# Performance work log

Measured on AMD Instinct MI355X. Metric: run time of the kernel, lower is better.

## Reference

```python
import jax, jax.numpy as jnp
import numpy as np

EPS = 1e-08


def setup_inputs() -> dict:
    key = jax.random.key(0)
    k1, k2 = jax.random.split(key)
    x = jax.random.normal(k1, (8192, 4096), dtype=jnp.float32)
    # xavier-uniform-ish init for weight (faithful scale; exact init irrelevant to math)
    limit = float(np.sqrt(6.0 / (4096 + 4096)))
    weight = jax.random.uniform(k2, (4096, 4096), dtype=jnp.float32, minval=-limit, maxval=limit)
    mask = jnp.ones((4096, 4096), dtype=jnp.float32)
    bias = jnp.zeros((4096,), dtype=jnp.float32)
    return {"x": x, "weight": weight, "mask": mask, "bias": bias}


def reference(x, weight, mask, bias):
    # masked weights
    mw = weight * mask  # [out, in]
    aw = jnp.abs(mw)
    # per-call global stats (training mode, adaptive threshold)
    scale = aw.mean() + EPS
    threshold = jnp.std(aw, ddof=1) * 0.5  # torch .std() is unbiased
    # ternary {-1, 0, +1} then rescale
    tern = jnp.where(mw > threshold, 1.0, 0.0) + jnp.where(mw < -threshold, -1.0, 0.0)
    tw = tern * scale
    # F.linear: x @ W^T + b
    return jnp.einsum("bi,oi->bo", x, tw) + bias
```

## Files before the change

kernel.cpp:

```cpp
#include <hip/hip_runtime.h>
#include <hip/hip_bf16.h>
#include <stdint.h>

#define M_DIM 8192
#define N_DIM 4096
#define K_DIM 4096
#define NW (N_DIM * K_DIM)

typedef __bf16 bf16x8 __attribute__((ext_vector_type(8)));
typedef float  floatx4 __attribute__((ext_vector_type(4)));
typedef unsigned short u16;
typedef unsigned int   u32;

__global__ void zero_stats(double* S) {
    if (threadIdx.x < 2) S[threadIdx.x] = 0.0;
}

__global__ void reduce_moments(const float* __restrict__ w,
                               const float* __restrict__ msk,
                               double* __restrict__ S) {
    const int nv = NW / 4;
    const int stride = gridDim.x * blockDim.x;
    int idx = blockIdx.x * blockDim.x + threadIdx.x;
    float s1 = 0.f, s2 = 0.f;
    const float4* w4 = (const float4*)w;
    const float4* m4 = (const float4*)msk;
    for (int i = idx; i < nv; i += stride) {
        float4 a = w4[i];
        float4 b = m4[i];
        float p0 = fabsf(a.x * b.x), p1 = fabsf(a.y * b.y);
        float p2 = fabsf(a.z * b.z), p3 = fabsf(a.w * b.w);
        s1 += p0 + p1 + p2 + p3;
        s2 += p0 * p0 + p1 * p1 + p2 * p2 + p3 * p3;
    }
    double d1 = (double)s1, d2 = (double)s2;
    #pragma unroll
    for (int off = 32; off > 0; off >>= 1) {
        d1 += __shfl_down(d1, off);
        d2 += __shfl_down(d2, off);
    }
    __shared__ double sh[8];
    int lane = threadIdx.x & 63;
    int wv = threadIdx.x >> 6;
    if (lane == 0) { sh[wv] = d1; sh[wv + 4] = d2; }
    __syncthreads();
    if (threadIdx.x == 0) {
        atomicAdd(&S[0], sh[0] + sh[1] + sh[2] + sh[3]);
        atomicAdd(&S[1], sh[4] + sh[5] + sh[6] + sh[7]);
    }
}

__global__ void finalize_stats(const double* __restrict__ S, float* __restrict__ st) {
    if (threadIdx.x == 0) {
        const double n = (double)NW;
        double s1 = S[0], s2 = S[1];
        double mean = s1 / n;
        double var = (s2 - s1 * s1 / n) / (n - 1.0);
        st[0] = (float)(mean + 1e-8);
        st[1] = (float)(0.5 * sqrt(var));
    }
}

__global__ void ternarize(const float* __restrict__ w, const float* __restrict__ msk,
                          const float* __restrict__ st, u16* __restrict__ tw) {
    const float thr = st[1];
    const int i = (blockIdx.x * blockDim.x + threadIdx.x) * 8;
    float4 a0 = *(const float4*)(w + i);
    float4 a1 = *(const float4*)(w + i + 4);
    float4 b0 = *(const float4*)(msk + i);
    float4 b1 = *(const float4*)(msk + i + 4);
    float p[8] = {a0.x * b0.x, a0.y * b0.y, a0.z * b0.z, a0.w * b0.w,
                  a1.x * b1.x, a1.y * b1.y, a1.z * b1.z, a1.w * b1.w};
    union { u16 u[8]; uint4 v; } r;
    #pragma unroll
    for (int j = 0; j < 8; ++j)
        r.u[j] = p[j] > thr ? (u16)0x3F80 : (p[j] < -thr ? (u16)0xBF80 : (u16)0);
    *(uint4*)(tw + i) = r.v;
}

__device__ __forceinline__ u16 f2bf(float f) {
    u32 u = __float_as_uint(f);
    u += 0x7FFFu + ((u >> 16) & 1u);
    return (u16)(u >> 16);
}

__global__ void cvt_x(const float* __restrict__ x, u16* __restrict__ y) {
    const int i = (blockIdx.x * blockDim.x + threadIdx.x) * 8;
    float4 a0 = *(const float4*)(x + i);
    float4 a1 = *(const float4*)(x + i + 4);
    union { u16 u[8]; uint4 v; } r;
    r.u[0] = f2bf(a0.x); r.u[1] = f2bf(a0.y); r.u[2] = f2bf(a0.z); r.u[3] = f2bf(a0.w);
    r.u[4] = f2bf(a1.x); r.u[5] = f2bf(a1.y); r.u[6] = f2bf(a1.z); r.u[7] = f2bf(a1.w);
    *(uint4*)(y + i) = r.v;
}

__device__ __forceinline__ void gld_lds16(const __bf16* g, __bf16* l) {
    __builtin_amdgcn_global_load_lds(
        (__attribute__((address_space(1))) void*)g,
        (__attribute__((address_space(3))) void*)l, 16, 0, 0);
}

__global__ __launch_bounds__(256) void gemm_tern(
        const __bf16* __restrict__ A, const __bf16* __restrict__ B,
        const float* __restrict__ bias, const float* __restrict__ st,
        float* __restrict__ C) {
    __shared__ __bf16 As[128 * 32];
    __shared__ __bf16 Bs[128 * 32];

    const int t = threadIdx.x;
    const int lane = t & 63;
    const int wv = t >> 6;
    const int wm = (wv >> 1) * 64;
    const int wn = (wv & 1) * 64;
    const int bm = blockIdx.y * 128;
    const int bn = blockIdx.x * 128;

    const int r  = t >> 2;
    const int kk = (t & 3) * 8;
    const __bf16* ga0 = A + (size_t)(bm + r) * K_DIM + kk;
    const __bf16* ga1 = A + (size_t)(bm + 64 + r) * K_DIM + kk;
    const __bf16* gb0 = B + (size_t)(bn + r) * K_DIM + kk;
    const __bf16* gb1 = B + (size_t)(bn + 64 + r) * K_DIM + kk;
    __bf16* la0 = As + t * 8;
    __bf16* la1 = As + 2048 + t * 8;
    __bf16* lb0 = Bs + t * 8;
    __bf16* lb1 = Bs + 2048 + t * 8;

    floatx4 acc[4][4] = {};

    const int mrow = lane & 15;
    const int kc = (lane >> 4) * 8;

    for (int k0 = 0; k0 < K_DIM; k0 += 32) {
        __syncthreads();
        gld_lds16(ga0 + k0, la0);
        gld_lds16(ga1 + k0, la1);
        gld_lds16(gb0 + k0, lb0);
        gld_lds16(gb1 + k0, lb1);
        __syncthreads();

        bf16x8 af[4], bfr[4];
        #pragma unroll
        for (int i = 0; i < 4; ++i) {
            af[i]  = *(const bf16x8*)(As + (wm + i * 16 + mrow) * 32 + kc);
            bfr[i] = *(const bf16x8*)(Bs + (wn + i * 16 + mrow) * 32 + kc);
        }
        #pragma unroll
        for (int im = 0; im < 4; ++im)
            #pragma unroll
            for (int in = 0; in < 4; ++in)
                acc[im][in] = __builtin_amdgcn_mfma_f32_16x16x32_bf16(
                    af[im], bfr[in], acc[im][in], 0, 0, 0);
    }

    const float scale = st[0];
    const int rbase = bm + wm + ((lane >> 4) << 2);
    const int cbase = bn + wn + (lane & 15);
    #pragma unroll
    for (int in = 0; in < 4; ++in) {
        const int col = cbase + in * 16;
        const float bv = bias[col];
        #pragma unroll
        for (int im = 0; im < 4; ++im) {
            const int row = rbase + im * 16;
            #pragma unroll
            for (int rg = 0; rg < 4; ++rg)
                C[(size_t)(row + rg) * N_DIM + col] = acc[im][in][rg] * scale + bv;
        }
    }
}

extern "C" void kernel_launch(void* const* d_in, const int* in_sizes, int n_in,
                              void* d_out, int out_size, void* d_ws, size_t ws_size,
                              hipStream_t stream) {
    const float* x    = (const float*)d_in[0];
    const float* w    = (const float*)d_in[1];
    const float* msk  = (const float*)d_in[2];
    const float* bias = (const float*)d_in[3];
    float* out = (float*)d_out;

    char* ws = (char*)d_ws;
    double* S   = (double*)ws;
    float*  st  = (float*)(ws + 64);
    u16*    tern = (u16*)(ws + 256);
    u16*    xbf  = (u16*)(ws + 256 + (size_t)NW * 2);

    zero_stats<<<1, 64, 0, stream>>>(S);
    reduce_moments<<<1024, 256, 0, stream>>>(w, msk, S);
    finalize_stats<<<1, 64, 0, stream>>>(S, st);
    ternarize<<<NW / (256 * 8), 256, 0, stream>>>(w, msk, st, tern);
    cvt_x<<<(M_DIM * K_DIM) / (256 * 8), 256, 0, stream>>>(x, xbf);

    dim3 grid(N_DIM / 128, M_DIM / 128);
    gemm_tern<<<grid, 256, 0, stream>>>((const __bf16*)xbf, (const __bf16*)tern,
                                        bias, st, out);
}
```

Baseline: 647.1 us.

## Fuse x conversion with moment reduction and replace atomics with partials

Merges the bf16 conversion of x and the weight moment reduction into one launch, where block index picks the role, so both memory-bound passes can run at the same time. The double atomics are replaced by per-block partial sums that a 256-thread finalize kernel reduces, and the zero_stats launch is removed. Partials reuse the ternary weight buffer's workspace region, which is safe because ternarize runs after finalize. This cuts two launches and lets the small reduction overlap the large conversion; the GEMM dominates, so the gain is limited.

After: 654.2 us. About the same (+1.1%).

```diff
diff --git a/kernel.cpp b/kernel.cpp
--- a/kernel.cpp
+++ b/kernel.cpp
@@ -7,53 +7,87 @@
 #define K_DIM 4096
 #define NW (N_DIM * K_DIM)
 
+#define CVT_BLOCKS 16384
+#define MOM_BLOCKS 2048
+
 typedef __bf16 bf16x8 __attribute__((ext_vector_type(8)));
 typedef float  floatx4 __attribute__((ext_vector_type(4)));
 typedef unsigned short u16;
 typedef unsigned int   u32;
 
-__global__ void zero_stats(double* S) {
-    if (threadIdx.x < 2) S[threadIdx.x] = 0.0;
-}
-
-__global__ void reduce_moments(const float* __restrict__ w,
-                               const float* __restrict__ msk,
-                               double* __restrict__ S) {
-    const int nv = NW / 4;
-    const int stride = gridDim.x * blockDim.x;
-    int idx = blockIdx.x * blockDim.x + threadIdx.x;
-    float s1 = 0.f, s2 = 0.f;
-    const float4* w4 = (const float4*)w;
-    const float4* m4 = (const float4*)msk;
-    for (int i = idx; i < nv; i += stride) {
-        float4 a = w4[i];
-        float4 b = m4[i];
-        float p0 = fabsf(a.x * b.x), p1 = fabsf(a.y * b.y);
-        float p2 = fabsf(a.z * b.z), p3 = fabsf(a.w * b.w);
-        s1 += p0 + p1 + p2 + p3;
-        s2 += p0 * p0 + p1 * p1 + p2 * p2 + p3 * p3;
-    }
-    double d1 = (double)s1, d2 = (double)s2;
+__device__ __forceinline__ u16 f2bf(float f) {
+    u32 u = __float_as_uint(f);
+    u += 0x7FFFu + ((u >> 16) & 1u);
+    return (u16)(u >> 16);
+}
+
+__global__ __launch_bounds__(256) void fused_pre(
+        const float* __restrict__ x, u16* __restrict__ xbf,
+        const float* __restrict__ w, const float* __restrict__ msk,
+        double* __restrict__ partials) {
+    __shared__ double sh[8];
+    const int b = blockIdx.x;
+    if (b < CVT_BLOCKS) {
+        const int i = (b * 256 + (int)threadIdx.x) * 8;
+        float4 a0 = *(const float4*)(x + i);
+        float4 a1 = *(const float4*)(x + i + 4);
+        union { u16 u[8]; uint4 v; } r;
+        r.u[0] = f2bf(a0.x); r.u[1] = f2bf(a0.y); r.u[2] = f2bf(a0.z); r.u[3] = f2bf(a0.w);
+        r.u[4] = f2bf(a1.x); r.u[5] = f2bf(a1.y); r.u[6] = f2bf(a1.z); r.u[7] = f2bf(a1.w);
+        *(uint4*)(xbf + i) = r.v;
+    } else {
+        const int mb = b - CVT_BLOCKS;
+        const int nv = NW / 4;
+        const int stride = MOM_BLOCKS * 256;
+        int idx = mb * 256 + (int)threadIdx.x;
+        float s1 = 0.f, s2 = 0.f;
+        const float4* w4 = (const float4*)w;
+        const float4* m4 = (const float4*)msk;
+        for (int i = idx; i < nv; i += stride) {
+            float4 a = w4[i];
+            float4 bb = m4[i];
+            float p0 = fabsf(a.x * bb.x), p1 = fabsf(a.y * bb.y);
+            float p2 = fabsf(a.z * bb.z), p3 = fabsf(a.w * bb.w);
+            s1 += p0 + p1 + p2 + p3;
+            s2 += p0 * p0 + p1 * p1 + p2 * p2 + p3 * p3;
+        }
+        double d1 = (double)s1, d2 = (double)s2;
+        #pragma unroll
+        for (int off = 32; off > 0; off >>= 1) {
+            d1 += __shfl_down(d1, off);
+            d2 += __shfl_down(d2, off);
+        }
+        int lane = threadIdx.x & 63;
+        int wv = threadIdx.x >> 6;
+        if (lane == 0) { sh[wv] = d1; sh[wv + 4] = d2; }
+        __syncthreads();
+        if (threadIdx.x == 0) {
+            partials[mb * 2]     = sh[0] + sh[1] + sh[2] + sh[3];
+            partials[mb * 2 + 1] = sh[4] + sh[5] + sh[6] + sh[7];
+        }
+    }
+}
+
+__global__ void finalize_stats(const double* __restrict__ partials, float* __restrict__ st) {
+    __shared__ double sh[8];
+    double d1 = 0.0, d2 = 0.0;
+    for (int i = threadIdx.x; i < MOM_BLOCKS; i += 256) {
+        d1 += partials[i * 2];
+        d2 += partials[i * 2 + 1];
+    }
     #pragma unroll
     for (int off = 32; off > 0; off >>= 1) {
         d1 += __shfl_down(d1, off);
         d2 += __shfl_down(d2, off);
     }
-    __shared__ double sh[8];
     int lane = threadIdx.x & 63;
     int wv = threadIdx.x >> 6;
     if (lane == 0) { sh[wv] = d1; sh[wv + 4] = d2; }
     __syncthreads();
     if (threadIdx.x == 0) {
-        atomicAdd(&S[0], sh[0] + sh[1] + sh[2] + sh[3]);
-        atomicAdd(&S[1], sh[4] + sh[5] + sh[6] + sh[7]);
-    }
-}
-
-__global__ void finalize_stats(const double* __restrict__ S, float* __restrict__ st) {
-    if (threadIdx.x == 0) {
+        double s1 = sh[0] + sh[1] + sh[2] + sh[3];
+        double s2 = sh[4] + sh[5] + sh[6] + sh[7];
         const double n = (double)NW;
-        double s1 = S[0], s2 = S[1];
         double mean = s1 / n;
         double var = (s2 - s1 * s1 / n) / (n - 1.0);
         st[0] = (float)(mean + 1e-8);
@@ -78,22 +112,6 @@
     *(uint4*)(tw + i) = r.v;
 }
 
-__device__ __forceinline__ u16 f2bf(float f) {
-    u32 u = __float_as_uint(f);
-    u += 0x7FFFu + ((u >> 16) & 1u);
-    return (u16)(u >> 16);
-}
-
-__global__ void cvt_x(const float* __restrict__ x, u16* __restrict__ y) {
-    const int i = (blockIdx.x * blockDim.x + threadIdx.x) * 8;
-    float4 a0 = *(const float4*)(x + i);
-    float4 a1 = *(const float4*)(x + i + 4);
-    union { u16 u[8]; uint4 v; } r;
-    r.u[0] = f2bf(a0.x); r.u[1] = f2bf(a0.y); r.u[2] = f2bf(a0.z); r.u[3] = f2bf(a0.w);
-    r.u[4] = f2bf(a1.x); r.u[5] = f2bf(a1.y); r.u[6] = f2bf(a1.z); r.u[7] = f2bf(a1.w);
-    *(uint4*)(y + i) = r.v;
-}
-
 __device__ __forceinline__ void gld_lds16(const __bf16* g, __bf16* l) {
     __builtin_amdgcn_global_load_lds(
         (__attribute__((address_space(1))) void*)g,
@@ -180,16 +198,14 @@
     float* out = (float*)d_out;
 
     char* ws = (char*)d_ws;
-    double* S   = (double*)ws;
-    float*  st  = (float*)(ws + 64);
-    u16*    tern = (u16*)(ws + 256);
-    u16*    xbf  = (u16*)(ws + 256 + (size_t)NW * 2);
-
-    zero_stats<<<1, 64, 0, stream>>>(S);
-    reduce_moments<<<1024, 256, 0, stream>>>(w, msk, S);
-    finalize_stats<<<1, 64, 0, stream>>>(S, st);
+    float*  st       = (float*)(ws + 64);
+    u16*    tern     = (u16*)(ws + 256);
+    double* partials = (double*)(ws + 256);
+    u16*    xbf      = (u16*)(ws + 256 + (size_t)NW * 2);
+
+    fused_pre<<<CVT_BLOCKS + MOM_BLOCKS, 256, 0, stream>>>(x, xbf, w, msk, partials);
+    finalize_stats<<<1, 256, 0, stream>>>(partials, st);
     ternarize<<<NW / (256 * 8), 256, 0, stream>>>(w, msk, st, tern);
-    cvt_x<<<(M_DIM * K_DIM) / (256 * 8), 256, 0, stream>>>(x, xbf);
 
     dim3 grid(N_DIM / 128, M_DIM / 128);
     gemm_tern<<<grid, 256, 0, stream>>>((const __bf16*)xbf, (const __bf16*)tern,
```
